# Optimization experiments

Hardware: AMD Instinct MI355X
Metric: run time of the kernel (lower is better)

Reference implementation:

```python
import jax, jax.numpy as jnp
import numpy as np
from jax import lax

IN_CH = 256
UP = 8
DN = ('NCHW', 'OIHW', 'NCHW')


def setup_inputs() -> dict:
    key = jax.random.key(0)
    ks = jax.random.split(key, 6)
    B, H, W = 8, 96, 96
    flow_lr = jax.random.normal(ks[0], (B, 2, H, W), dtype=jnp.float32)
    feat = jax.random.normal(ks[1], (B, IN_CH, H, W), dtype=jnp.float32)
    w1 = jax.random.normal(ks[2], (IN_CH, IN_CH, 3, 3), dtype=jnp.float32) * 0.02
    b1 = jnp.zeros((IN_CH,), dtype=jnp.float32)
    w2 = jax.random.normal(ks[3], (UP * UP * 9, IN_CH, 1, 1), dtype=jnp.float32) * 0.02
    b2 = jnp.zeros((UP * UP * 9,), dtype=jnp.float32)
    return {"flow_lr": flow_lr, "feat": feat, "w1": w1, "b1": b1, "w2": w2, "b2": b2}


def reference(flow_lr, feat, w1, b1, w2, b2):
    B, _, H, W = flow_lr.shape
    up = UP
    # mask head: 3x3 conv + relu + 1x1 conv
    x = lax.conv_general_dilated(feat, w1, (1, 1), 'SAME', dimension_numbers=DN)
    x = jax.nn.relu(x + b1[None, :, None, None])
    mask = lax.conv_general_dilated(x, w2, (1, 1), 'SAME', dimension_numbers=DN)
    mask = mask + b2[None, :, None, None]
    # channel dim 9*up*up splits as (9, up, up), matching torch .view(B,1,9,up,up,H,W)
    mask = mask.reshape(B, 9, up, up, H, W)
    mask = jax.nn.softmax(mask, axis=1)
    # unfold(flow_lr, 3, padding=1): 9 zero-padded 3x3 shifts, row-major (kh, kw)
    pad = jnp.pad(flow_lr, ((0, 0), (0, 0), (1, 1), (1, 1)))
    flow_unf = jnp.stack(
        [pad[:, :, i:i + H, j:j + W] for i in range(3) for j in range(3)], axis=2
    )  # (B, 2, 9, H, W)
    # convex combination over the 9 neighbors
    up_flow = jnp.einsum('bkpqhw,bckhw->bcpqhw', mask, flow_unf)  # (B,2,up,up,H,W)
    # pixel-shuffle: (B,2,p,q,H,W) -> (B,2,H,p,W,q) -> (B,2,H*up,W*up)
    up_flow = up_flow.transpose(0, 1, 4, 2, 5, 3).reshape(B, 2, H * up, W * up)
    return up_flow * up
```

## Files before the change

kernel.cpp:

```cpp
#include <hip/hip_runtime.h>
#include <hip/hip_bf16.h>
#include <stdint.h>

typedef unsigned short u16;
typedef __bf16 bf16x8 __attribute__((ext_vector_type(8)));
typedef float f32x4 __attribute__((ext_vector_type(4)));

#define MFMA16(a, b, c) __builtin_amdgcn_mfma_f32_16x16x32_bf16((a), (b), (c), 0, 0, 0)

#define GLOAD16(g, l)                                                        \
  __builtin_amdgcn_global_load_lds(                                          \
      (const __attribute__((address_space(1))) void*)(g),                    \
      (__attribute__((address_space(3))) void*)(l), 16, 0, 0)

static __device__ __forceinline__ u16 f2bf(float f) {
  union { float f; uint32_t u; } v;
  v.f = f;
  uint32_t u = v.u;
  return (u16)((u + 0x7FFFu + ((u >> 16) & 1u)) >> 16);
}
static __device__ __forceinline__ float u2f(uint32_t u) {
  union { uint32_t u; float f; } v;
  v.u = u;
  return v.f;
}

#define FEATT_ELEMS (8u * 98u * 98u * 256u)
#define W1T_OFF     FEATT_ELEMS
#define W1T_ELEMS   (256u * 2304u)
#define W2B_OFF     (W1T_OFF + W1T_ELEMS)
#define W2B_ELEMS   (576u * 256u)
#define X_OFF       (W2B_OFF + W2B_ELEMS)

__global__ __launch_bounds__(256) void prep_all(const float* __restrict__ feat,
                                                const float* __restrict__ w1,
                                                const float* __restrict__ w2,
                                                u16* __restrict__ featT,
                                                u16* __restrict__ w1t,
                                                u16* __restrict__ w2b) {
  const int blk = blockIdx.x;
  const int t = threadIdx.x;
  if (blk < 388) {
    int tid = blk * 256 + t;
    int b = tid / (388 * 32);
    int rem = tid % (388 * 32);
    int pos = rem >> 5, v = rem & 31;
    int h, w;
    if (pos < 98) { h = 0; w = pos; }
    else if (pos < 196) { h = 97; w = pos - 98; }
    else if (pos < 292) { h = pos - 196 + 1; w = 0; }
    else { h = pos - 292 + 1; w = 97; }
    uint4* dst = (uint4*)(featT + (size_t)((b * 98 + h) * 98 + w) * 256 + v * 8);
    *dst = make_uint4(0, 0, 0, 0);
  } else if (blk < 4996) {
    int idx = blk - 388;
    int pt = idx % 144, ct = (idx / 144) & 3, b = idx / 576;
    const int p0 = pt * 64, c0 = ct * 64;
    __shared__ float tile[64][65];
    const int pj = t & 63, ci0 = t >> 6;
#pragma unroll
    for (int r = 0; r < 16; ++r) {
      int ci = r * 4 + ci0;
      tile[ci][pj] = feat[(b * 256 + c0 + ci) * 9216 + p0 + pj];
    }
    __syncthreads();
    const int pl = t >> 2, cc0 = (t & 3) * 16;
    const int pix = p0 + pl;
    const int h = pix / 96, w = pix % 96;
    uint32_t u[8];
#pragma unroll
    for (int i = 0; i < 8; ++i) {
      u16 lo = f2bf(tile[cc0 + 2 * i][pl]);
      u16 hi = f2bf(tile[cc0 + 2 * i + 1][pl]);
      u[i] = (uint32_t)lo | ((uint32_t)hi << 16);
    }
    uint4* dst = (uint4*)(featT + (size_t)((b * 98 + h + 1) * 98 + (w + 1)) * 256 + c0 + cc0);
    dst[0] = make_uint4(u[0], u[1], u[2], u[3]);
    dst[1] = make_uint4(u[4], u[5], u[6], u[7]);
  } else {
    int i = (blk - 4996) * 256 + t;
    if (i < 589824) {
      int oc = i / 2304, r = i % 2304;
      int tap = r >> 8, cin = r & 255;
      w1t[i] = f2bf(w1[(oc * 256 + cin) * 9 + tap]);
    } else {
      int j = i - 589824;
      if (j < 147456) w2b[j] = f2bf(w2[j]);
    }
  }
}

__global__ __launch_bounds__(512, 4) void gemm1(const u16* __restrict__ featT,
                                                const u16* __restrict__ w1t,
                                                const float* __restrict__ b1,
                                                u16* __restrict__ xout) {
  __shared__ __align__(16) u16 sA[128 * 64];
  __shared__ __align__(16) u16 sB[256 * 64];
  __shared__ float sb1[256];

  const int t = threadIdx.x;
  const int wave = t >> 6, lane = t & 63;
  const int bid = blockIdx.x;
  const int mt = (bid & 7) * 72 + (bid >> 3);
  const int b = mt / 72;
  const int ip0 = (mt % 72) * 128;

  if (t < 256) sb1[t] = b1[t];

  const u16* aBase[2];
  const u16* bBase[4];
#pragma unroll
  for (int r = 0; r < 2; ++r) {
    int row = r * 64 + wave * 8 + (lane >> 3);
    int chunk = (lane & 7) ^ (row & 7);
    int ip = ip0 + row;
    int h = ip / 96, w = ip % 96;
    aBase[r] = featT + (size_t)((b * 98 + h + 1) * 98 + (w + 1)) * 256 + chunk * 8;
  }
#pragma unroll
  for (int r = 0; r < 4; ++r) {
    int row = wave * 32 + r * 8 + (lane >> 3);
    int chunk = (lane & 7) ^ (row & 7);
    bBase[r] = w1t + (size_t)row * 2304 + chunk * 8;
  }

  const int wm = wave >> 2, wn = wave & 3;
  int aoffs[4][2], boffs[4][2];
#pragma unroll
  for (int m = 0; m < 4; ++m) {
#pragma unroll
    for (int ki = 0; ki < 2; ++ki) {
      int kc = ki * 4 + (lane >> 4);
      int rowa = wm * 64 + m * 16 + (lane & 15);
      aoffs[m][ki] = rowa * 64 + ((kc ^ (rowa & 7)) * 8);
      int rowb = wn * 64 + m * 16 + (lane & 15);
      boffs[m][ki] = rowb * 64 + ((kc ^ (rowb & 7)) * 8);
    }
  }

  f32x4 acc[4][4];
#pragma unroll
  for (int m = 0; m < 4; ++m)
#pragma unroll
    for (int n = 0; n < 4; ++n) acc[m][n] = f32x4{0.f, 0.f, 0.f, 0.f};

  for (int kt = 0; kt < 36; ++kt) {
    int tap = kt >> 2;
    int dh = tap / 3 - 1, dw = tap % 3 - 1;
    int aoff = (dh * 98 + dw) * 256 + (kt & 3) * 64;
    int boff = kt * 64;
#pragma unroll
    for (int r = 0; r < 2; ++r) GLOAD16(aBase[r] + aoff, &sA[(r * 64 + wave * 8) * 64]);
#pragma unroll
    for (int r = 0; r < 4; ++r) GLOAD16(bBase[r] + boff, &sB[(wave * 32 + r * 8) * 64]);
    __syncthreads();
#pragma unroll
    for (int ki = 0; ki < 2; ++ki) {
      bf16x8 av[4], bv[4];
#pragma unroll
      for (int m = 0; m < 4; ++m) av[m] = *(const bf16x8*)&sA[aoffs[m][ki]];
#pragma unroll
      for (int n = 0; n < 4; ++n) bv[n] = *(const bf16x8*)&sB[boffs[n][ki]];
#pragma unroll
      for (int m = 0; m < 4; ++m)
#pragma unroll
        for (int n = 0; n < 4; ++n) acc[m][n] = MFMA16(av[m], bv[n], acc[m][n]);
    }
    __syncthreads();
  }

  const int pix0g = mt * 128;
#pragma unroll
  for (int m = 0; m < 4; ++m) {
    int pixl = wm * 64 + m * 16 + ((lane >> 4) << 2);
#pragma unroll
    for (int n = 0; n < 4; ++n) {
      int oc = wn * 64 + n * 16 + (lane & 15);
      float bias = sb1[oc];
      f32x4 v = acc[m][n];
#pragma unroll
      for (int j = 0; j < 4; ++j) {
        float val = v[j] + bias;
        val = val > 0.f ? val : 0.f;
        xout[(size_t)(pix0g + pixl + j) * 256 + oc] = f2bf(val);
      }
    }
  }
}

__global__ __launch_bounds__(512) void gemm2fq(const u16* __restrict__ xws,
                                               const u16* __restrict__ w2b,
                                               const float* __restrict__ b2g,
                                               const float* __restrict__ flow,
                                               float* __restrict__ out) {
  __shared__ __align__(16) u16 sW[2][9216];
  __shared__ uint32_t sFlowP[1152];
  __shared__ float sb2f[576];

  const int t = threadIdx.x;
  const int wave = t >> 6, lane = t & 63;
  const int bid = blockIdx.x;
  const int mt = (bid & 7) * 72 + (bid >> 3);
  const int b = mt / 72;
  const int ipl0 = (mt % 72) * 128;
  const int l15 = lane & 15, kc = lane >> 4;

  auto stageQ = [&](int u, int bufi) {
    int cI = u >> 2, kq = u & 3;
    if (t < 384) {
#pragma unroll
      for (int pass = 0; pass < 3; ++pass) {
        int c = pass * 384 + t;
        int n = c >> 3, cl = c & 7;
        int cg = cl ^ (n & 7);
        int chan = (n >> 4) * 64 + cI * 16 + (n & 15);
        GLOAD16(w2b + (size_t)chan * 256 + kq * 64 + cg * 8,
                &sW[bufi][(pass * 384 + wave * 64) * 8]);
      }
    }
  };
  stageQ(0, 0);

  for (int i = t; i < 1152; i += 512) {
    int nf = i >> 7, p = i & 127;
    int ip = ipl0 + p;
    int h = ip / 96, w = ip % 96;
    int hh = h + nf / 3 - 1, ww = w + nf % 3 - 1;
    float vx = 0.f, vy = 0.f;
    if (hh >= 0 && hh < 96 && ww >= 0 && ww < 96) {
      vx = flow[b * 18432 + hh * 96 + ww];
      vy = flow[b * 18432 + 9216 + hh * 96 + ww];
    }
    sFlowP[i] = (uint32_t)f2bf(vx) | ((uint32_t)f2bf(vy) << 16);
  }
  for (int i = t; i < 576; i += 512) sb2f[i] = b2g[i];

  const int px = wave * 16 + l15;
  const u16* xr = &xws[((size_t)mt * 128 + px) * 256];
  bf16x8 areg[8];
#pragma unroll
  for (int s = 0; s < 8; ++s) areg[s] = *(const bf16x8*)&xr[(s * 4 + kc) * 8];

  const int iph = (ipl0 + px) / 96, ipw = (ipl0 + px) % 96;
  const size_t ob = ((size_t)(b * 2) * 768 + iph * 8) * 768 + ipw * 8;
  const int q0 = (kc & 1) * 4, pk = kc >> 1;

  uint32_t fp[9];
  f32x4 acc[9];
#pragma unroll
  for (int u = 0; u < 16; ++u) {
    __syncthreads();
    if (u == 0) {
#pragma unroll
      for (int nf = 0; nf < 9; ++nf) fp[nf] = sFlowP[nf * 128 + px];
    }
    if (u < 15) stageQ(u + 1, (u + 1) & 1);
    const int cI = u >> 2, kq = u & 3;
    if (kq == 0) {
#pragma unroll
      for (int nf = 0; nf < 9; ++nf) acc[nf] = f32x4{0.f, 0.f, 0.f, 0.f};
    }
    const u16* base = sW[u & 1];
    __builtin_amdgcn_s_setprio(1);
#pragma unroll
    for (int ki = 0; ki < 2; ++ki) {
      bf16x8 a = areg[kq * 2 + ki];
      int kcc = ki * 4 + kc;
#pragma unroll
      for (int nf = 0; nf < 9; ++nf) {
        int n = nf * 16 + l15;
        bf16x8 wv = *(const bf16x8*)&base[n * 64 + ((kcc ^ (n & 7)) * 8)];
        acc[nf] = MFMA16(wv, a, acc[nf]);
      }
    }
    __builtin_amdgcn_s_setprio(0);
    if (kq == 3) {
      f32x4 vx4, vy4;
#pragma unroll
      for (int j = 0; j < 4; ++j) {
        int pql = kc * 4 + j;
        float v[9], mx = -3.0e38f;
#pragma unroll
        for (int nf = 0; nf < 9; ++nf) {
          v[nf] = acc[nf][j] + sb2f[nf * 64 + cI * 16 + pql];
          mx = fmaxf(mx, v[nf]);
        }
        float ssum = 0.f, fx = 0.f, fy = 0.f;
#pragma unroll
        for (int nf = 0; nf < 9; ++nf) {
          float e = __expf(v[nf] - mx);
          ssum += e;
          fx += e * u2f(fp[nf] << 16);
          fy += e * u2f(fp[nf] & 0xFFFF0000u);
        }
        float sc = 8.0f / ssum;
        vx4[j] = fx * sc;
        vy4[j] = fy * sc;
      }
      int p = cI * 2 + pk;
      *(f32x4*)&out[ob + (size_t)p * 768 + q0] = vx4;
      *(f32x4*)&out[ob + 589824 + (size_t)p * 768 + q0] = vy4;
    }
  }
}

extern "C" void kernel_launch(void* const* d_in, const int* in_sizes, int n_in,
                              void* d_out, int out_size, void* d_ws, size_t ws_size,
                              hipStream_t stream) {
  const float* flow = (const float*)d_in[0];
  const float* feat = (const float*)d_in[1];
  const float* w1 = (const float*)d_in[2];
  const float* b1 = (const float*)d_in[3];
  const float* w2 = (const float*)d_in[4];
  const float* b2 = (const float*)d_in[5];
  float* out = (float*)d_out;
  u16* ws = (u16*)d_ws;
  u16* featT = ws;
  u16* w1t = ws + W1T_OFF;
  u16* w2b = ws + W2B_OFF;
  u16* xws = ws + X_OFF;

  prep_all<<<7876, 256, 0, stream>>>(feat, w1, w2, featT, w1t, w2b);
  gemm1<<<576, 512, 0, stream>>>(featT, w1t, b1, xws);
  gemm2fq<<<576, 512, 0, stream>>>(xws, w2b, b2, flow, out);
}
```

Baseline: 185.7 us.

## Double-buffer gemm1 LDS tiles and drop softmax max subtraction

New measurement: 198.3 us. +6.8%, slower.

```diff
diff --git a/kernel.cpp b/kernel.cpp
--- a/kernel.cpp
+++ b/kernel.cpp
@@ -90,12 +90,11 @@
   }
 }
 
-__global__ __launch_bounds__(512, 4) void gemm1(const u16* __restrict__ featT,
-                                                const u16* __restrict__ w1t,
-                                                const float* __restrict__ b1,
-                                                u16* __restrict__ xout) {
-  __shared__ __align__(16) u16 sA[128 * 64];
-  __shared__ __align__(16) u16 sB[256 * 64];
+__global__ __launch_bounds__(512, 4) void gemm1p(const u16* __restrict__ featT,
+                                                 const u16* __restrict__ w1t,
+                                                 const float* __restrict__ b1,
+                                                 u16* __restrict__ xout) {
+  __shared__ __align__(16) u16 smem[2 * 12288];
   __shared__ float sb1[256];
 
   const int t = threadIdx.x;
@@ -107,35 +106,45 @@
 
   if (t < 256) sb1[t] = b1[t];
 
-  const u16* aBase[2];
-  const u16* bBase[4];
+  const u16* aSrc;
+  {
+    int rowA = wave * 16 + (lane >> 2);
+    int jA = (lane & 3) ^ (rowA & 3);
+    int ip = ip0 + rowA;
+    int h = ip / 96, w = ip % 96;
+    aSrc = featT + (size_t)((b * 98 + h + 1) * 98 + (w + 1)) * 256 + jA * 8;
+  }
+  const u16* bSrc[2];
 #pragma unroll
   for (int r = 0; r < 2; ++r) {
-    int row = r * 64 + wave * 8 + (lane >> 3);
-    int chunk = (lane & 7) ^ (row & 7);
-    int ip = ip0 + row;
-    int h = ip / 96, w = ip % 96;
-    aBase[r] = featT + (size_t)((b * 98 + h + 1) * 98 + (w + 1)) * 256 + chunk * 8;
-  }
-#pragma unroll
-  for (int r = 0; r < 4; ++r) {
-    int row = wave * 32 + r * 8 + (lane >> 3);
-    int chunk = (lane & 7) ^ (row & 7);
-    bBase[r] = w1t + (size_t)row * 2304 + chunk * 8;
-  }
+    int rowB = wave * 32 + r * 16 + (lane >> 2);
+    int jB = (lane & 3) ^ (rowB & 3);
+    bSrc[r] = w1t + (size_t)rowB * 2304 + jB * 8;
+  }
+
+  auto stage = [&](int kt, int bufi) {
+    int tap = kt >> 3;
+    int dh = tap / 3 - 1, dw = tap % 3 - 1;
+    int aoff = (dh * 98 + dw) * 256 + (kt & 7) * 32;
+    int boff = kt * 32;
+    u16* base = &smem[bufi * 12288];
+    GLOAD16(aSrc + aoff, base + wave * 512);
+    GLOAD16(bSrc[0] + boff, base + 4096 + wave * 1024);
+    GLOAD16(bSrc[1] + boff, base + 4096 + wave * 1024 + 512);
+  };
 
   const int wm = wave >> 2, wn = wave & 3;
-  int aoffs[4][2], boffs[4][2];
+  const int l15 = lane & 15, kcc = lane >> 4;
+  int aoffs[4], boffs[4];
 #pragma unroll
   for (int m = 0; m < 4; ++m) {
-#pragma unroll
-    for (int ki = 0; ki < 2; ++ki) {
-      int kc = ki * 4 + (lane >> 4);
-      int rowa = wm * 64 + m * 16 + (lane & 15);
-      aoffs[m][ki] = rowa * 64 + ((kc ^ (rowa & 7)) * 8);
-      int rowb = wn * 64 + m * 16 + (lane & 15);
-      boffs[m][ki] = rowb * 64 + ((kc ^ (rowb & 7)) * 8);
-    }
+    int rowa = wm * 64 + m * 16 + l15;
+    aoffs[m] = rowa * 32 + ((kcc ^ (rowa & 3)) * 8);
+  }
+#pragma unroll
+  for (int n = 0; n < 4; ++n) {
+    int rowb = wn * 64 + n * 16 + l15;
+    boffs[n] = 4096 + rowb * 32 + ((kcc ^ (rowb & 3)) * 8);
   }
 
   f32x4 acc[4][4];
@@ -144,29 +153,23 @@
 #pragma unroll
     for (int n = 0; n < 4; ++n) acc[m][n] = f32x4{0.f, 0.f, 0.f, 0.f};
 
-  for (int kt = 0; kt < 36; ++kt) {
-    int tap = kt >> 2;
-    int dh = tap / 3 - 1, dw = tap % 3 - 1;
-    int aoff = (dh * 98 + dw) * 256 + (kt & 3) * 64;
-    int boff = kt * 64;
-#pragma unroll
-    for (int r = 0; r < 2; ++r) GLOAD16(aBase[r] + aoff, &sA[(r * 64 + wave * 8) * 64]);
-#pragma unroll
-    for (int r = 0; r < 4; ++r) GLOAD16(bBase[r] + boff, &sB[(wave * 32 + r * 8) * 64]);
+  stage(0, 0);
+  __syncthreads();
+  int buf = 0;
+  for (int kt = 0; kt < 72; ++kt) {
+    if (kt < 71) stage(kt + 1, buf ^ 1);
+    const u16* base = &smem[buf * 12288];
+    bf16x8 av[4], bv[4];
+#pragma unroll
+    for (int m = 0; m < 4; ++m) av[m] = *(const bf16x8*)&base[aoffs[m]];
+#pragma unroll
+    for (int n = 0; n < 4; ++n) bv[n] = *(const bf16x8*)&base[boffs[n]];
+#pragma unroll
+    for (int m = 0; m < 4; ++m)
+#pragma unroll
+      for (int n = 0; n < 4; ++n) acc[m][n] = MFMA16(av[m], bv[n], acc[m][n]);
     __syncthreads();
-#pragma unroll
-    for (int ki = 0; ki < 2; ++ki) {
-      bf16x8 av[4], bv[4];
-#pragma unroll
-      for (int m = 0; m < 4; ++m) av[m] = *(const bf16x8*)&sA[aoffs[m][ki]];
-#pragma unroll
-      for (int n = 0; n < 4; ++n) bv[n] = *(const bf16x8*)&sB[boffs[n][ki]];
-#pragma unroll
-      for (int m = 0; m < 4; ++m)
-#pragma unroll
-        for (int n = 0; n < 4; ++n) acc[m][n] = MFMA16(av[m], bv[n], acc[m][n]);
-    }
-    __syncthreads();
+    buf ^= 1;
   }
 
   const int pix0g = mt * 128;
@@ -175,7 +178,7 @@
     int pixl = wm * 64 + m * 16 + ((lane >> 4) << 2);
 #pragma unroll
     for (int n = 0; n < 4; ++n) {
-      int oc = wn * 64 + n * 16 + (lane & 15);
+      int oc = wn * 64 + n * 16 + l15;
       float bias = sb1[oc];
       f32x4 v = acc[m][n];
 #pragma unroll
@@ -279,16 +282,10 @@
 #pragma unroll
       for (int j = 0; j < 4; ++j) {
         int pql = kc * 4 + j;
-        float v[9], mx = -3.0e38f;
+        float ssum = 0.f, fx = 0.f, fy = 0.f;
 #pragma unroll
         for (int nf = 0; nf < 9; ++nf) {
-          v[nf] = acc[nf][j] + sb2f[nf * 64 + cI * 16 + pql];
-          mx = fmaxf(mx, v[nf]);
-        }
-        float ssum = 0.f, fx = 0.f, fy = 0.f;
-#pragma unroll
-        for (int nf = 0; nf < 9; ++nf) {
-          float e = __expf(v[nf] - mx);
+          float e = __expf(acc[nf][j] + sb2f[nf * 64 + cI * 16 + pql]);
           ssum += e;
           fx += e * u2f(fp[nf] << 16);
           fy += e * u2f(fp[nf] & 0xFFFF0000u);
@@ -321,6 +318,6 @@
   u16* xws = ws + X_OFF;
 
   prep_all<<<7876, 256, 0, stream>>>(feat, w1, w2, featT, w1t, w2b);
-  gemm1<<<576, 512, 0, stream>>>(featT, w1t, b1, xws);
+  gemm1p<<<576, 512, 0, stream>>>(featT, w1t, b1, xws);
   gemm2fq<<<576, 512, 0, stream>>>(xws, w2b, b2, flow, out);
 }
```
